# Performance work log

Hardware: AMD Instinct MI355X
Metric: run time of the kernel (lower is better)

Reference implementation:

```python
import jax, jax.numpy as jnp
import numpy as np

TAGSET = 64
START_TAG = 62
STOP_TAG = 63
B, S = 32, 256


def setup_inputs() -> dict:
    key = jax.random.key(0)
    k1, k2, k3 = jax.random.split(key, 3)
    features = jax.random.normal(k1, (B, S, TAGSET, TAGSET), dtype=jnp.float32)
    targets = jax.random.randint(k2, (B, S), 0, TAGSET * TAGSET, dtype=jnp.int64)
    lengths = jax.random.randint(k3, (B,), 1, S + 1, dtype=jnp.int64)
    # pack_padded_sequence requires lengths sorted descending; ensure max length = S
    lengths = jnp.sort(lengths)[::-1].at[0].set(S)
    return {"features": features, "targets": targets, "lengths": lengths}


def reference(features, targets, lengths):
    Bc, Sc, T, _ = features.shape
    # --- gold score: gather the score of the true (from_tag, to_tag) pair per token ---
    flat = features.reshape(Bc, Sc, T * T)                       # [B,S,T*T]
    scores_at_targets = jnp.take_along_axis(flat, targets[:, :, None], axis=2)[..., 0]
    valid = (jnp.arange(Sc)[None, :] < lengths[:, None])          # [B,S] pad mask
    gold_score = jnp.sum(jnp.where(valid, scores_at_targets, 0.0))

    # --- CRF forward algorithm (log-sum-exp recurrence over time) ---
    init = features[:, 0, START_TAG, :]                           # [B,T] (all lengths >= 1)
    feats_t = jnp.swapaxes(features, 0, 1)[1:]                    # [S-1,B,T,T]
    active = (jnp.arange(1, Sc)[:, None] < lengths[None, :])       # [S-1,B]

    def step(scores, inp):
        feat, act = inp                                           # feat [B,T,T], act [B]
        new = jax.nn.logsumexp(feat + scores[:, :, None], axis=1)  # lse over from-tag
        scores = jnp.where(act[:, None], new, scores)
        return scores, None

    scores_upto_t, _ = jax.lax.scan(step, init, (feats_t, active))
    all_paths_scores = jnp.sum(scores_upto_t[:, STOP_TAG])

    return (all_paths_scores - gold_score) / Bc
```

## Files before the change

### kernel.cpp

```cpp
#include <hip/hip_runtime.h>
#include <cmath>

#define NB 32
#define NS 256
#define NT 64
#define START_TAG 62
#define STOP_TAG 63
#define CL 8
#define NCH 32
#define GS 8.0f
#define LOG64 4.1588830833596715f
#define LDP 68

#define CMAT_BYTES ((size_t)NB * NCH * NT * NT * 2)

__device__ inline unsigned short f2bf(float x) {
  unsigned u = __float_as_uint(x);
  u += 0x7fffu + ((u >> 16) & 1u);
  return (unsigned short)(u >> 16);
}

__global__ __launch_bounds__(256) void chunk_kernel(
    const float* __restrict__ feat, const int* __restrict__ lengths,
    unsigned int* __restrict__ cmat) {
  const int b = blockIdx.x;
  const int c = blockIdx.y;
  const int len = lengths[b];
  const int t1 = 1 + c * CL;
  const int nmat = min(len, t1 + CL) - t1;
  if (nmat <= 0) return;

  __shared__ float At[2][NT][LDP];
  __shared__ float Em[NT][NT];

  const int tid = threadIdx.x;
  const float* fb = feat + ((size_t)b * NS + t1) * (NT * NT);

  const int sj = tid & 15;
  const int sk = tid >> 4;

  #pragma unroll
  for (int r = 0; r < 4; ++r) {
    const int row = sk + 16 * r;
    float4 f4 = *(const float4*)(fb + row * NT + 4 * sj);
    At[0][4 * sj + 0][row] = __expf(f4.x - GS);
    At[0][4 * sj + 1][row] = __expf(f4.y - GS);
    At[0][4 * sj + 2][row] = __expf(f4.z - GS);
    At[0][4 * sj + 3][row] = __expf(f4.w - GS);
  }

  float4 raw[4];
  if (nmat > 1) {
    #pragma unroll
    for (int r = 0; r < 4; ++r)
      raw[r] = *(const float4*)(fb + (size_t)(NT * NT) + (sk + 16 * r) * NT + 4 * sj);
  }
  __syncthreads();

  const int it = tid & 15;
  const int jt = tid >> 4;
  int p = 0;

  for (int k = 1; k < nmat; ++k) {
    #pragma unroll
    for (int r = 0; r < 4; ++r) {
      const int row = sk + 16 * r;
      float4 e4;
      e4.x = __expf(raw[r].x - GS);
      e4.y = __expf(raw[r].y - GS);
      e4.z = __expf(raw[r].z - GS);
      e4.w = __expf(raw[r].w - GS);
      *(float4*)&Em[row][4 * sj] = e4;
    }
    __syncthreads();

    if (k + 1 < nmat) {
      #pragma unroll
      for (int r = 0; r < 4; ++r)
        raw[r] = *(const float4*)(fb + (size_t)(k + 1) * (NT * NT) +
                                  (sk + 16 * r) * NT + 4 * sj);
    }

    float acc[4][4] = {};
    #pragma unroll 4
    for (int kk = 0; kk < NT; ++kk) {
      float4 a4 = *(const float4*)&At[p][kk][4 * it];
      float4 m4 = *(const float4*)&Em[kk][4 * jt];
      acc[0][0] = fmaf(a4.x, m4.x, acc[0][0]);
      acc[0][1] = fmaf(a4.x, m4.y, acc[0][1]);
      acc[0][2] = fmaf(a4.x, m4.z, acc[0][2]);
      acc[0][3] = fmaf(a4.x, m4.w, acc[0][3]);
      acc[1][0] = fmaf(a4.y, m4.x, acc[1][0]);
      acc[1][1] = fmaf(a4.y, m4.y, acc[1][1]);
      acc[1][2] = fmaf(a4.y, m4.z, acc[1][2]);
      acc[1][3] = fmaf(a4.y, m4.w, acc[1][3]);
      acc[2][0] = fmaf(a4.z, m4.x, acc[2][0]);
      acc[2][1] = fmaf(a4.z, m4.y, acc[2][1]);
      acc[2][2] = fmaf(a4.z, m4.z, acc[2][2]);
      acc[2][3] = fmaf(a4.z, m4.w, acc[2][3]);
      acc[3][0] = fmaf(a4.w, m4.x, acc[3][0]);
      acc[3][1] = fmaf(a4.w, m4.y, acc[3][1]);
      acc[3][2] = fmaf(a4.w, m4.z, acc[3][2]);
      acc[3][3] = fmaf(a4.w, m4.w, acc[3][3]);
    }

    #pragma unroll
    for (int cc = 0; cc < 4; ++cc) {
      float4 w;
      w.x = acc[0][cc] * 0.015625f;
      w.y = acc[1][cc] * 0.015625f;
      w.z = acc[2][cc] * 0.015625f;
      w.w = acc[3][cc] * 0.015625f;
      *(float4*)&At[1 - p][4 * jt + cc][4 * it] = w;
    }
    __syncthreads();
    p ^= 1;
  }

  const int row = tid >> 2;
  const int cg = tid & 3;
  unsigned int ub[8];
  #pragma unroll
  for (int u = 0; u < 8; ++u) {
    float v0 = At[p][row][16 * cg + 2 * u];
    float v1 = At[p][row][16 * cg + 2 * u + 1];
    ub[u] = (unsigned)f2bf(v0) | ((unsigned)f2bf(v1) << 16);
  }
  unsigned int* dst = cmat + ((size_t)b * NCH + c) * 2048 + row * 32 + cg * 8;
  *(uint4*)dst = make_uint4(ub[0], ub[1], ub[2], ub[3]);
  *((uint4*)dst + 1) = make_uint4(ub[4], ub[5], ub[6], ub[7]);
}

__global__ __launch_bounds__(64) void combine_kernel(
    const float* __restrict__ feat, const int* __restrict__ lengths,
    const unsigned int* __restrict__ cmat, float* __restrict__ res) {
  const int b = blockIdx.x;
  const int j = threadIdx.x;
  __shared__ float sv[NT];
  const int len = lengths[b];
  const float* f0 = feat + (size_t)b * NS * (NT * NT);

  float x = f0[START_TAG * NT + j];
  float m = x;
  #pragma unroll
  for (int off = 32; off; off >>= 1) m = fmaxf(m, __shfl_xor(m, off));
  float v = __expf(x - m);
  float L = m;

  const int nch = (len - 1 + CL - 1) / CL;
  uint4 Q0[8];
  if (nch > 0) {
    const uint4* P = (const uint4*)cmat + (size_t)b * NCH * 512 + j * 8;
    #pragma unroll
    for (int w = 0; w < 8; ++w) Q0[w] = P[w];
  }

  for (int c2 = 0; c2 < nch; ++c2) {
    sv[j] = v;
    __builtin_amdgcn_wave_barrier();

    uint4 Q1[8];
    if (c2 + 1 < nch) {
      const uint4* P = (const uint4*)cmat + ((size_t)b * NCH + c2 + 1) * 512 + j * 8;
      #pragma unroll
      for (int w = 0; w < 8; ++w) Q1[w] = P[w];
    }

    float acc = 0.f;
    const float4* svp = (const float4*)sv;
    #pragma unroll
    for (int w = 0; w < 8; ++w) {
      uint4 q = Q0[w];
      float4 s0 = svp[2 * w], s1 = svp[2 * w + 1];
      acc = fmaf(__uint_as_float(q.x << 16), s0.x, acc);
      acc = fmaf(__uint_as_float(q.x & 0xffff0000u), s0.y, acc);
      acc = fmaf(__uint_as_float(q.y << 16), s0.z, acc);
      acc = fmaf(__uint_as_float(q.y & 0xffff0000u), s0.w, acc);
      acc = fmaf(__uint_as_float(q.z << 16), s1.x, acc);
      acc = fmaf(__uint_as_float(q.z & 0xffff0000u), s1.y, acc);
      acc = fmaf(__uint_as_float(q.w << 16), s1.z, acc);
      acc = fmaf(__uint_as_float(q.w & 0xffff0000u), s1.w, acc);
    }
    __builtin_amdgcn_wave_barrier();

    const int tt1 = 1 + c2 * CL;
    const int nmat = min(len, tt1 + CL) - tt1;
    L += (float)nmat * GS + (float)(nmat - 1) * LOG64;

    float mm = acc;
    #pragma unroll
    for (int off = 32; off; off >>= 1) mm = fmaxf(mm, __shfl_xor(mm, off));
    v = acc / mm;
    L += __logf(mm);

    #pragma unroll
    for (int w = 0; w < 8; ++w) Q0[w] = Q1[w];
  }

  float lv = __logf(v);
  float path = L + __shfl(lv, STOP_TAG);
  if (j == 0) res[b] = path;
}

__global__ __launch_bounds__(256) void gold_kernel(
    const float* __restrict__ feat, const int* __restrict__ targets,
    const int* __restrict__ lengths, float* __restrict__ res) {
  int idx = blockIdx.x * 256 + threadIdx.x;
  int b = idx >> 8;
  int s = idx & 255;
  float v = 0.0f;
  if (s < lengths[b]) {
    int tgt = targets[idx];
    v = feat[(size_t)idx * (NT * NT) + tgt];
  }
  #pragma unroll
  for (int off = 32; off; off >>= 1) v += __shfl_down(v, off);
  if ((threadIdx.x & 63) == 0) atomicAdd(&res[NB], v);
}

__global__ void finalize_kernel(const float* __restrict__ res,
                                float* __restrict__ out) {
  int l = threadIdx.x;
  float v = (l < NB) ? res[l] : 0.f;
  #pragma unroll
  for (int off = 32; off; off >>= 1) v += __shfl_down(v, off);
  if (l == 0) out[0] = (v - res[NB]) * (1.0f / (float)NB);
}

extern "C" void kernel_launch(void* const* d_in, const int* in_sizes, int n_in,
                              void* d_out, int out_size, void* d_ws, size_t ws_size,
                              hipStream_t stream) {
  const float* feat    = (const float*)d_in[0];
  const int*   targets = (const int*)d_in[1];
  const int*   lengths = (const int*)d_in[2];
  unsigned int* cmat = (unsigned int*)d_ws;
  float* res = (float*)((char*)d_ws + CMAT_BYTES);
  float* out = (float*)d_out;

  hipMemsetAsync(res + NB, 0, sizeof(float), stream);
  gold_kernel<<<NB, 256, 0, stream>>>(feat, targets, lengths, res);
  chunk_kernel<<<dim3(NB, NCH), 256, 0, stream>>>(feat, lengths, cmat);
  combine_kernel<<<NB, 64, 0, stream>>>(feat, lengths, cmat, res);
  finalize_kernel<<<1, 64, 0, stream>>>(res, out);
}
```

Baseline: 242.2 us.

## Use bf16 MFMA for chunk matrix products and fuse gold/finalize into combine

The chunk kernel's 64x64 fp32 FMA matrix products are replaced by bf16 MFMA 16x16x32 instructions, with the exponentiated inputs stored as packed bf16 in shared memory and the raw feature prefetch double-buffered. The gold-score gather and the final reduction move into the combine kernel, which atomically accumulates into the output, removing two kernel launches. This cuts FMA work and launch overhead, at the cost of reduced precision in the intermediate products (bf16 instead of fp32) and an atomic accumulation whose order is nondeterministic.

```diff
diff --git a/kernel.cpp b/kernel.cpp
--- a/kernel.cpp
+++ b/kernel.cpp
@@ -10,14 +10,20 @@
 #define NCH 32
 #define GS 8.0f
 #define LOG64 4.1588830833596715f
-#define LDP 68
-
-#define CMAT_BYTES ((size_t)NB * NCH * NT * NT * 2)
+#define SP 66
+
+typedef __attribute__((ext_vector_type(8))) short short8;
+typedef __attribute__((ext_vector_type(4))) float float4v;
+
+union FragU { unsigned u[4]; short8 s; };
 
 __device__ inline unsigned short f2bf(float x) {
   unsigned u = __float_as_uint(x);
   u += 0x7fffu + ((u >> 16) & 1u);
   return (unsigned short)(u >> 16);
+}
+__device__ inline unsigned pack2(float a, float b) {
+  return (unsigned)f2bf(a) | ((unsigned)f2bf(b) << 16);
 }
 
 __global__ __launch_bounds__(256) void chunk_kernel(
@@ -30,115 +36,134 @@
   const int nmat = min(len, t1 + CL) - t1;
   if (nmat <= 0) return;
 
-  __shared__ float At[2][NT][LDP];
-  __shared__ float Em[NT][NT];
+  __shared__ unsigned short Pb[2][NT * SP];
+  __shared__ unsigned short Et[2][NT * SP];
 
   const int tid = threadIdx.x;
   const float* fb = feat + ((size_t)b * NS + t1) * (NT * NT);
 
-  const int sj = tid & 15;
-  const int sk = tid >> 4;
-
-  #pragma unroll
-  for (int r = 0; r < 4; ++r) {
-    const int row = sk + 16 * r;
-    float4 f4 = *(const float4*)(fb + row * NT + 4 * sj);
-    At[0][4 * sj + 0][row] = __expf(f4.x - GS);
-    At[0][4 * sj + 1][row] = __expf(f4.y - GS);
-    At[0][4 * sj + 2][row] = __expf(f4.z - GS);
-    At[0][4 * sj + 3][row] = __expf(f4.w - GS);
-  }
-
-  float4 raw[4];
+  {
+    const int cj = tid & 15, rk = tid >> 4;
+    #pragma unroll
+    for (int r = 0; r < 4; ++r) {
+      const int row = rk + 16 * r;
+      float4 f4 = *(const float4*)(fb + row * NT + 4 * cj);
+      unsigned* dst = (unsigned*)&Pb[0][row * SP + 4 * cj];
+      dst[0] = pack2(__expf(f4.x - GS), __expf(f4.y - GS));
+      dst[1] = pack2(__expf(f4.z - GS), __expf(f4.w - GS));
+    }
+  }
+
+  const int sj = tid & 15, r0 = tid >> 4;
+  float4 raw[2][4];
   if (nmat > 1) {
-    #pragma unroll
-    for (int r = 0; r < 4; ++r)
-      raw[r] = *(const float4*)(fb + (size_t)(NT * NT) + (sk + 16 * r) * NT + 4 * sj);
+    const float* p = fb + (NT * NT);
+    raw[1][0] = *(const float4*)(p + (2 * r0     ) * NT + 4 * sj);
+    raw[1][1] = *(const float4*)(p + (2 * r0 +  1) * NT + 4 * sj);
+    raw[1][2] = *(const float4*)(p + (2 * r0 + 32) * NT + 4 * sj);
+    raw[1][3] = *(const float4*)(p + (2 * r0 + 33) * NT + 4 * sj);
   }
   __syncthreads();
 
-  const int it = tid & 15;
-  const int jt = tid >> 4;
-  int p = 0;
+  const int lane = tid & 63, wv = tid >> 6;
+  const int ln = lane & 15, q = lane >> 4;
+  const int m0 = 16 * wv;
+  int pp = 0;
 
   for (int k = 1; k < nmat; ++k) {
-    #pragma unroll
-    for (int r = 0; r < 4; ++r) {
-      const int row = sk + 16 * r;
-      float4 e4;
-      e4.x = __expf(raw[r].x - GS);
-      e4.y = __expf(raw[r].y - GS);
-      e4.z = __expf(raw[r].z - GS);
-      e4.w = __expf(raw[r].w - GS);
-      *(float4*)&Em[row][4 * sj] = e4;
+    const int pf = k & 1;
+    if (k + 1 < nmat) {
+      const float* p = fb + (size_t)(k + 1) * (NT * NT);
+      raw[1 - pf][0] = *(const float4*)(p + (2 * r0     ) * NT + 4 * sj);
+      raw[1 - pf][1] = *(const float4*)(p + (2 * r0 +  1) * NT + 4 * sj);
+      raw[1 - pf][2] = *(const float4*)(p + (2 * r0 + 32) * NT + 4 * sj);
+      raw[1 - pf][3] = *(const float4*)(p + (2 * r0 + 33) * NT + 4 * sj);
+    }
+    {
+      unsigned short* et = Et[pf];
+      const float* r0p = (const float*)&raw[pf][0];
+      const float* r1p = (const float*)&raw[pf][1];
+      const float* r2p = (const float*)&raw[pf][2];
+      const float* r3p = (const float*)&raw[pf][3];
+      #pragma unroll
+      for (int cc = 0; cc < 4; ++cc) {
+        const int j = 4 * sj + cc;
+        *(unsigned*)&et[j * SP + 2 * r0] =
+            pack2(__expf(r0p[cc] - GS), __expf(r1p[cc] - GS));
+        *(unsigned*)&et[j * SP + 2 * r0 + 32] =
+            pack2(__expf(r2p[cc] - GS), __expf(r3p[cc] - GS));
+      }
     }
     __syncthreads();
 
-    if (k + 1 < nmat) {
+    FragU a0, a1;
+    const unsigned* ap = (const unsigned*)&Pb[pp][(m0 + ln) * SP];
+    a0.u[0] = ap[4 * q + 0]; a0.u[1] = ap[4 * q + 1];
+    a0.u[2] = ap[4 * q + 2]; a0.u[3] = ap[4 * q + 3];
+    a1.u[0] = ap[16 + 4 * q + 0]; a1.u[1] = ap[16 + 4 * q + 1];
+    a1.u[2] = ap[16 + 4 * q + 2]; a1.u[3] = ap[16 + 4 * q + 3];
+
+    float4v acc[4];
+    #pragma unroll
+    for (int tc = 0; tc < 4; ++tc) {
+      FragU b0, b1;
+      const unsigned* bp = (const unsigned*)&Et[pf][(16 * tc + ln) * SP];
+      b0.u[0] = bp[4 * q + 0]; b0.u[1] = bp[4 * q + 1];
+      b0.u[2] = bp[4 * q + 2]; b0.u[3] = bp[4 * q + 3];
+      b1.u[0] = bp[16 + 4 * q + 0]; b1.u[1] = bp[16 + 4 * q + 1];
+      b1.u[2] = bp[16 + 4 * q + 2]; b1.u[3] = bp[16 + 4 * q + 3];
+      float4v z = {0.f, 0.f, 0.f, 0.f};
+      acc[tc] = __builtin_amdgcn_mfma_f32_16x16x32_bf16(a0.s, b0.s, z, 0, 0, 0);
+      acc[tc] = __builtin_amdgcn_mfma_f32_16x16x32_bf16(a1.s, b1.s, acc[tc], 0, 0, 0);
+    }
+
+    unsigned short* pn = Pb[1 - pp];
+    #pragma unroll
+    for (int tc = 0; tc < 4; ++tc) {
       #pragma unroll
-      for (int r = 0; r < 4; ++r)
-        raw[r] = *(const float4*)(fb + (size_t)(k + 1) * (NT * NT) +
-                                  (sk + 16 * r) * NT + 4 * sj);
-    }
-
-    float acc[4][4] = {};
-    #pragma unroll 4
-    for (int kk = 0; kk < NT; ++kk) {
-      float4 a4 = *(const float4*)&At[p][kk][4 * it];
-      float4 m4 = *(const float4*)&Em[kk][4 * jt];
-      acc[0][0] = fmaf(a4.x, m4.x, acc[0][0]);
-      acc[0][1] = fmaf(a4.x, m4.y, acc[0][1]);
-      acc[0][2] = fmaf(a4.x, m4.z, acc[0][2]);
-      acc[0][3] = fmaf(a4.x, m4.w, acc[0][3]);
-      acc[1][0] = fmaf(a4.y, m4.x, acc[1][0]);
-      acc[1][1] = fmaf(a4.y, m4.y, acc[1][1]);
-      acc[1][2] = fmaf(a4.y, m4.z, acc[1][2]);
-      acc[1][3] = fmaf(a4.y, m4.w, acc[1][3]);
-      acc[2][0] = fmaf(a4.z, m4.x, acc[2][0]);
-      acc[2][1] = fmaf(a4.z, m4.y, acc[2][1]);
-      acc[2][2] = fmaf(a4.z, m4.z, acc[2][2]);
-      acc[2][3] = fmaf(a4.z, m4.w, acc[2][3]);
-      acc[3][0] = fmaf(a4.w, m4.x, acc[3][0]);
-      acc[3][1] = fmaf(a4.w, m4.y, acc[3][1]);
-      acc[3][2] = fmaf(a4.w, m4.z, acc[3][2]);
-      acc[3][3] = fmaf(a4.w, m4.w, acc[3][3]);
-    }
-
-    #pragma unroll
-    for (int cc = 0; cc < 4; ++cc) {
-      float4 w;
-      w.x = acc[0][cc] * 0.015625f;
-      w.y = acc[1][cc] * 0.015625f;
-      w.z = acc[2][cc] * 0.015625f;
-      w.w = acc[3][cc] * 0.015625f;
-      *(float4*)&At[1 - p][4 * jt + cc][4 * it] = w;
-    }
-    __syncthreads();
-    p ^= 1;
-  }
-
-  const int row = tid >> 2;
-  const int cg = tid & 3;
-  unsigned int ub[8];
-  #pragma unroll
-  for (int u = 0; u < 8; ++u) {
-    float v0 = At[p][row][16 * cg + 2 * u];
-    float v1 = At[p][row][16 * cg + 2 * u + 1];
-    ub[u] = (unsigned)f2bf(v0) | ((unsigned)f2bf(v1) << 16);
-  }
-  unsigned int* dst = cmat + ((size_t)b * NCH + c) * 2048 + row * 32 + cg * 8;
-  *(uint4*)dst = make_uint4(ub[0], ub[1], ub[2], ub[3]);
-  *((uint4*)dst + 1) = make_uint4(ub[4], ub[5], ub[6], ub[7]);
+      for (int rg = 0; rg < 4; ++rg) {
+        const int row = m0 + 4 * q + rg;
+        pn[row * SP + 16 * tc + ln] = f2bf(acc[tc][rg] * 0.015625f);
+      }
+    }
+    pp ^= 1;
+  }
+  __syncthreads();
+
+  {
+    const int j = tid >> 2, cg = tid & 3;
+    unsigned ub[8];
+    #pragma unroll
+    for (int u = 0; u < 8; ++u) {
+      unsigned short lo = Pb[pp][(16 * cg + 2 * u    ) * SP + j];
+      unsigned short hi = Pb[pp][(16 * cg + 2 * u + 1) * SP + j];
+      ub[u] = (unsigned)lo | ((unsigned)hi << 16);
+    }
+    unsigned* dst = cmat + ((size_t)b * NCH + c) * 2048 + j * 32 + cg * 8;
+    *(uint4*)dst       = make_uint4(ub[0], ub[1], ub[2], ub[3]);
+    *((uint4*)dst + 1) = make_uint4(ub[4], ub[5], ub[6], ub[7]);
+  }
 }
 
 __global__ __launch_bounds__(64) void combine_kernel(
-    const float* __restrict__ feat, const int* __restrict__ lengths,
-    const unsigned int* __restrict__ cmat, float* __restrict__ res) {
+    const float* __restrict__ feat, const int* __restrict__ targets,
+    const int* __restrict__ lengths, const unsigned int* __restrict__ cmat,
+    float* __restrict__ out) {
   const int b = blockIdx.x;
   const int j = threadIdx.x;
   __shared__ float sv[NT];
   const int len = lengths[b];
   const float* f0 = feat + (size_t)b * NS * (NT * NT);
+
+  float gold = 0.f;
+  #pragma unroll
+  for (int g = 0; g < 4; ++g) {
+    const int s = j + 64 * g;
+    if (s < len) {
+      const int tgt = targets[b * NS + s];
+      gold += f0[(size_t)s * (NT * NT) + tgt];
+    }
+  }
 
   float x = f0[START_TAG * NT + j];
   float m = x;
@@ -170,16 +195,16 @@
     const float4* svp = (const float4*)sv;
     #pragma unroll
     for (int w = 0; w < 8; ++w) {
-      uint4 q = Q0[w];
+      uint4 qq = Q0[w];
       float4 s0 = svp[2 * w], s1 = svp[2 * w + 1];
-      acc = fmaf(__uint_as_float(q.x << 16), s0.x, acc);
-      acc = fmaf(__uint_as_float(q.x & 0xffff0000u), s0.y, acc);
-      acc = fmaf(__uint_as_float(q.y << 16), s0.z, acc);
-      acc = fmaf(__uint_as_float(q.y & 0xffff0000u), s0.w, acc);
-      acc = fmaf(__uint_as_float(q.z << 16), s1.x, acc);
-      acc = fmaf(__uint_as_float(q.z & 0xffff0000u), s1.y, acc);
-      acc = fmaf(__uint_as_float(q.w << 16), s1.z, acc);
-      acc = fmaf(__uint_as_float(q.w & 0xffff0000u), s1.w, acc);
+      acc = fmaf(__uint_as_float(qq.x << 16), s0.x, acc);
+      acc = fmaf(__uint_as_float(qq.x & 0xffff0000u), s0.y, acc);
+      acc = fmaf(__uint_as_float(qq.y << 16), s0.z, acc);
+      acc = fmaf(__uint_as_float(qq.y & 0xffff0000u), s0.w, acc);
+      acc = fmaf(__uint_as_float(qq.z << 16), s1.x, acc);
+      acc = fmaf(__uint_as_float(qq.z & 0xffff0000u), s1.y, acc);
+      acc = fmaf(__uint_as_float(qq.w << 16), s1.z, acc);
+      acc = fmaf(__uint_as_float(qq.w & 0xffff0000u), s1.w, acc);
     }
     __builtin_amdgcn_wave_barrier();
 
@@ -199,32 +224,10 @@
 
   float lv = __logf(v);
   float path = L + __shfl(lv, STOP_TAG);
-  if (j == 0) res[b] = path;
-}
-
-__global__ __launch_bounds__(256) void gold_kernel(
-    const float* __restrict__ feat, const int* __restrict__ targets,
-    const int* __restrict__ lengths, float* __restrict__ res) {
-  int idx = blockIdx.x * 256 + threadIdx.x;
-  int b = idx >> 8;
-  int s = idx & 255;
-  float v = 0.0f;
-  if (s < lengths[b]) {
-    int tgt = targets[idx];
-    v = feat[(size_t)idx * (NT * NT) + tgt];
-  }
+
   #pragma unroll
-  for (int off = 32; off; off >>= 1) v += __shfl_down(v, off);
-  if ((threadIdx.x & 63) == 0) atomicAdd(&res[NB], v);
-}
-
-__global__ void finalize_kernel(const float* __restrict__ res,
-                                float* __restrict__ out) {
-  int l = threadIdx.x;
-  float v = (l < NB) ? res[l] : 0.f;
-  #pragma unroll
-  for (int off = 32; off; off >>= 1) v += __shfl_down(v, off);
-  if (l == 0) out[0] = (v - res[NB]) * (1.0f / (float)NB);
+  for (int off = 32; off; off >>= 1) gold += __shfl_down(gold, off);
+  if (j == 0) atomicAdd(out, (path - gold) * (1.0f / (float)NB));
 }
 
 extern "C" void kernel_launch(void* const* d_in, const int* in_sizes, int n_in,
@@ -234,12 +237,9 @@
   const int*   targets = (const int*)d_in[1];
   const int*   lengths = (const int*)d_in[2];
   unsigned int* cmat = (unsigned int*)d_ws;
-  float* res = (float*)((char*)d_ws + CMAT_BYTES);
   float* out = (float*)d_out;
 
-  hipMemsetAsync(res + NB, 0, sizeof(float), stream);
-  gold_kernel<<<NB, 256, 0, stream>>>(feat, targets, lengths, res);
+  hipMemsetAsync(d_out, 0, sizeof(float), stream);
   chunk_kernel<<<dim3(NB, NCH), 256, 0, stream>>>(feat, lengths, cmat);
-  combine_kernel<<<NB, 64, 0, stream>>>(feat, lengths, cmat, res);
-  finalize_kernel<<<1, 64, 0, stream>>>(res, out);
-}
+  combine_kernel<<<NB, 64, 0, stream>>>(feat, targets, lengths, cmat, out);
+}
```

After: 240.9 us. About the same (-0.5%).
